# Kernel optimization log

Measured on AMD Instinct MI355X. Metric: run time of the kernel, lower is better.

## Reference

```python
import jax, jax.numpy as jnp
import numpy as np

N, C, H, W = 128, 1024, 16, 16
D_IN, L, D_OUT, NQ = 2048, 512, 1024, 16


def setup_inputs() -> dict:
    key = jax.random.key(0)
    k1, k2, k3, k4, k5 = jax.random.split(key, 5)
    return {
        "cat_tensor": jax.random.normal(k1, (N, C, H, W), dtype=jnp.float32),
        "context": jax.random.normal(k2, (N, D_IN, L), dtype=jnp.float32),
        "query": jax.random.normal(k3, (1, NQ, D_IN), dtype=jnp.float32),
        "W_in": jax.random.normal(k4, (D_IN, D_IN), dtype=jnp.float32) * (1.0 / np.sqrt(D_IN)),
        "W_out": jax.random.normal(k5, (D_OUT, 2 * D_IN), dtype=jnp.float32) * (1.0 / np.sqrt(2 * D_IN)),
    }


def reference(cat_tensor, context, query, W_in, W_out):
    n, c, h, w = cat_tensor.shape
    # AttnBlock: context comes in as [N, D_in, L] -> transpose to [N, L, D_in]
    ctx = jnp.swapaxes(context, 1, 2)  # [N, L, D]
    # learned query broadcast over batch, then 'general' projection (Linear, no bias)
    q = jnp.einsum('nqd,ed->nqe', jnp.broadcast_to(query, (n,) + query.shape[1:]), W_in)  # [N, Q, D]
    scores = jnp.einsum('nqd,nld->nql', q, ctx)            # [N, Q, L]
    weights = jax.nn.softmax(scores, axis=-1)              # [N, Q, L]
    mix = jnp.einsum('nql,nld->nqd', weights, ctx)         # [N, Q, D]
    combined = jnp.concatenate([mix, q], axis=-1)          # [N, Q, 2D]
    out = jnp.tanh(jnp.einsum('nqe,oe->nqo', combined, W_out))  # [N, Q, D_out]
    # reshape queries to a small spatial map: [N, D_out, Hq, Hq]
    hq = int(np.sqrt(out.shape[1]))
    amap = jnp.swapaxes(out, 1, 2).reshape(n, out.shape[2], hq, hq)
    # F.interpolate(..., (H, W)) default mode='nearest': idx = floor(i * in / out)
    ih = (jnp.arange(h) * hq) // h
    iw = (jnp.arange(w) * hq) // w
    amap = amap[:, :, ih, :][:, :, :, iw]                  # [N, D_out, H, W]
    return jnp.concatenate([cat_tensor, amap], axis=1)     # [N, C + D_out, H, W]
```

## Files before the change

### kernel.cpp

```cpp
#include <hip/hip_runtime.h>
#include <hip/hip_bf16.h>

#define NB   128
#define CIN  1024
#define HW   256
#define DIN  2048
#define LL   512
#define DOUT 1024
#define NQ   16

typedef __attribute__((ext_vector_type(8))) short bf16x8;
typedef __attribute__((ext_vector_type(4))) float f32x4;

__global__ __launch_bounds__(256) void k_q(const float* __restrict__ query,
                                           const float* __restrict__ Win,
                                           float* __restrict__ qT) {
  int idx  = blockIdx.x * 4 + (threadIdx.x >> 6);
  int lane = threadIdx.x & 63;
  int e = idx >> 4, qi = idx & 15;
  const float* wr = Win + (size_t)e * DIN;
  const float* qr = query + (size_t)qi * DIN;
  float acc = 0.f;
  for (int d = lane; d < DIN; d += 64) acc += wr[d] * qr[d];
  #pragma unroll
  for (int m = 32; m; m >>= 1) acc += __shfl_xor(acc, m);
  if (lane == 0) qT[e * 16 + qi] = acc;
}

__global__ __launch_bounds__(256) void k_qfill(const float* __restrict__ qT,
                                               __hip_bfloat16* __restrict__ comb) {
  int idx = blockIdx.x * 256 + threadIdx.x;
  int m = idx >> 11, e = idx & 2047;
  comb[(size_t)m * (2 * DIN) + DIN + e] = __float2bfloat16(qT[e * 16 + (m & 15)]);
}

__global__ __launch_bounds__(256) void k_wcast(const float* __restrict__ W,
                                               __hip_bfloat16* __restrict__ Wb) {
  int idx = blockIdx.x * 256 + threadIdx.x;
  Wb[idx] = __float2bfloat16(W[idx]);
}

__global__ __launch_bounds__(256) void k_scores(const float* __restrict__ ctx,
                                                const float* __restrict__ qT,
                                                float* __restrict__ part) {
  int n = blockIdx.x, c = blockIdx.y, t = threadIdx.x;
  const float* cn  = ctx + (size_t)n * DIN * LL + (size_t)c * 512 * LL;
  const float* qTc = qT + (size_t)c * 512 * 16;
  float2 acc[16];
  #pragma unroll
  for (int qi = 0; qi < 16; ++qi) acc[qi] = make_float2(0.f, 0.f);
  #pragma unroll 4
  for (int d = 0; d < 512; ++d) {
    float2 v = *(const float2*)&cn[(size_t)d * LL + 2 * t];
    const float* qr = qTc + d * 16;
    #pragma unroll
    for (int qi = 0; qi < 16; ++qi) {
      acc[qi].x += qr[qi] * v.x;
      acc[qi].y += qr[qi] * v.y;
    }
  }
  float* po = part + (size_t)(c * NB + n) * 16 * LL;
  #pragma unroll
  for (int qi = 0; qi < 16; ++qi)
    *(float2*)&po[qi * LL + 2 * t] = acc[qi];
}

__global__ __launch_bounds__(256) void k_softmax(const float* __restrict__ part,
                                                 float* __restrict__ wT) {
  int b = blockIdx.x, n = b >> 4, qi = b & 15, t = threadIdx.x;
  __shared__ float red[256];
  float sc0 = 0.f, sc1 = 0.f;
  #pragma unroll
  for (int c = 0; c < 4; ++c) {
    const float* p = part + ((size_t)(c * NB + n) * 16 + qi) * LL;
    sc0 += p[t];
    sc1 += p[t + 256];
  }
  red[t] = fmaxf(sc0, sc1);
  __syncthreads();
  for (int s = 128; s; s >>= 1) { if (t < s) red[t] = fmaxf(red[t], red[t + s]); __syncthreads(); }
  float M = red[0];
  __syncthreads();
  float e0 = expf(sc0 - M), e1 = expf(sc1 - M);
  red[t] = e0 + e1;
  __syncthreads();
  for (int s = 128; s; s >>= 1) { if (t < s) red[t] += red[t + s]; __syncthreads(); }
  float inv = 1.0f / red[0];
  wT[((size_t)n * LL + t) * 16 + qi]       = e0 * inv;
  wT[((size_t)n * LL + t + 256) * 16 + qi] = e1 * inv;
}

__global__ __launch_bounds__(256) void k_mix(const float* __restrict__ ctx,
                                             const float* __restrict__ wT,
                                             __hip_bfloat16* __restrict__ comb) {
  int dt = blockIdx.x, n = blockIdx.y, t = threadIdx.x;
  int dbase = dt * 256;
  __shared__ float tile[256 * 33];
  const float* cn = ctx + (size_t)n * DIN * LL;
  const float* wn = wT + (size_t)n * LL * 16;
  float acc[16];
  #pragma unroll
  for (int qi = 0; qi < 16; ++qi) acc[qi] = 0.f;

  for (int ch = 0; ch < 16; ++ch) {
    int l0 = ch * 32;
    __syncthreads();
    int lq = (t & 7) * 4;
    #pragma unroll
    for (int p = 0; p < 8; ++p) {
      int row = (t >> 3) + p * 32;
      float4 g = *(const float4*)&cn[(size_t)(dbase + row) * LL + l0 + lq];
      float* dst = &tile[row * 33 + lq];
      dst[0] = g.x; dst[1] = g.y; dst[2] = g.z; dst[3] = g.w;
    }
    __syncthreads();
    for (int l = 0; l < 32; ++l) {
      float v = tile[t * 33 + l];
      const float* wr = wn + (size_t)(l0 + l) * 16;
      #pragma unroll
      for (int qi = 0; qi < 16; ++qi) acc[qi] += wr[qi] * v;
    }
  }
  #pragma unroll
  for (int qi = 0; qi < 16; ++qi)
    comb[(size_t)(n * 16 + qi) * (2 * DIN) + dbase + t] = __float2bfloat16(acc[qi]);
}

__global__ __launch_bounds__(256) void k_gemm(const __hip_bfloat16* __restrict__ A,
                                              const __hip_bfloat16* __restrict__ B,
                                              float* __restrict__ out) {
  __shared__ short la[64 * 40];
  __shared__ short lb[64 * 40];
  int t = threadIdx.x, lane = t & 63, wid = t >> 6;
  int m0 = blockIdx.y * 64, o0 = blockIdx.x * 64;
  int wy = wid >> 1, wx = wid & 1;
  f32x4 acc[2][2] = {};
  int srow = t >> 2, sq = (t & 3) * 8;
  const short* As = (const short*)A;
  const short* Bs = (const short*)B;

  for (int kc = 0; kc < 2 * DIN; kc += 32) {
    __syncthreads();
    *(float4*)&la[srow * 40 + sq] = *(const float4*)&As[(size_t)(m0 + srow) * (2 * DIN) + kc + sq];
    *(float4*)&lb[srow * 40 + sq] = *(const float4*)&Bs[(size_t)(o0 + srow) * (2 * DIN) + kc + sq];
    __syncthreads();
    int fr = lane & 15, fq = (lane >> 4) * 8;
    bf16x8 a0 = *(const bf16x8*)&la[(wy * 32 + fr) * 40 + fq];
    bf16x8 a1 = *(const bf16x8*)&la[(wy * 32 + 16 + fr) * 40 + fq];
    bf16x8 b0 = *(const bf16x8*)&lb[(wx * 32 + fr) * 40 + fq];
    bf16x8 b1 = *(const bf16x8*)&lb[(wx * 32 + 16 + fr) * 40 + fq];
    acc[0][0] = __builtin_amdgcn_mfma_f32_16x16x32_bf16(a0, b0, acc[0][0], 0, 0, 0);
    acc[0][1] = __builtin_amdgcn_mfma_f32_16x16x32_bf16(a0, b1, acc[0][1], 0, 0, 0);
    acc[1][0] = __builtin_amdgcn_mfma_f32_16x16x32_bf16(a1, b0, acc[1][0], 0, 0, 0);
    acc[1][1] = __builtin_amdgcn_mfma_f32_16x16x32_bf16(a1, b1, acc[1][1], 0, 0, 0);
  }

  int col = lane & 15, rbase = (lane >> 4) * 4;
  #pragma unroll
  for (int si = 0; si < 2; ++si)
    #pragma unroll
    for (int sj = 0; sj < 2; ++sj)
      #pragma unroll
      for (int r = 0; r < 4; ++r) {
        int m = m0 + wy * 32 + si * 16 + rbase + r;
        int o = o0 + wx * 32 + sj * 16 + col;
        float v = tanhf(acc[si][sj][r]);
        int n = m >> 4, qi = m & 15;
        float* op = out + (size_t)(n * 2048 + CIN + o) * HW
                        + ((qi >> 2) * 4) * 16 + (qi & 3) * 4;
        float4 vv = make_float4(v, v, v, v);
        *(float4*)&op[0]  = vv;
        *(float4*)&op[16] = vv;
        *(float4*)&op[32] = vv;
        *(float4*)&op[48] = vv;
      }
}

__global__ __launch_bounds__(256) void k_copy(const float* __restrict__ cat,
                                              float* __restrict__ out) {
  size_t idx = (size_t)blockIdx.x * 256 + threadIdx.x;
  int n = (int)(idx >> 16);
  int rem = (int)(idx & 65535);
  const float4* c4 = (const float4*)cat;
  float4* o4 = (float4*)out;
  o4[(size_t)n * 131072 + rem] = c4[idx];
}

extern "C" void kernel_launch(void* const* d_in, const int* in_sizes, int n_in,
                              void* d_out, int out_size, void* d_ws, size_t ws_size,
                              hipStream_t stream) {
  const float* cat   = (const float*)d_in[0];
  const float* ctx   = (const float*)d_in[1];
  const float* query = (const float*)d_in[2];
  const float* W_in  = (const float*)d_in[3];
  const float* W_out = (const float*)d_in[4];
  float* out = (float*)d_out;

  float* qT   = (float*)d_ws;
  float* wT   = qT + 32768;
  float* part = wT + 1048576;
  __hip_bfloat16* Wb   = (__hip_bfloat16*)(part + 4194304);
  __hip_bfloat16* comb = Wb + 4194304;

  k_q      <<<8192, 256, 0, stream>>>(query, W_in, qT);
  k_wcast  <<<16384, 256, 0, stream>>>(W_out, Wb);
  k_qfill  <<<16384, 256, 0, stream>>>(qT, comb);
  k_scores <<<dim3(128, 4), 256, 0, stream>>>(ctx, qT, part);
  k_softmax<<<2048, 256, 0, stream>>>(part, wT);
  k_mix    <<<dim3(8, 128), 256, 0, stream>>>(ctx, wT, comb);
  k_gemm   <<<dim3(16, 32), 256, 0, stream>>>(comb, Wb, out);
  k_copy   <<<32768, 256, 0, stream>>>(cat, out);
}
```

Baseline: 1.145 ms.

## Vectorize prep kernels, split scores over more chunks, prefetch tiles in mix and GEMM

k_q now computes all 16 queries per warp so each W_in row is read once, and k_wcast/k_qfill write eight bf16 values per thread with vector stores. k_scores splits the D reduction into 8 chunks instead of 4, doubling the block count for better occupancy at the cost of a larger partial-score buffer and more work in softmax. k_mix and k_gemm register-prefetch the next global tile while computing on the current LDS tile, overlapping load latency with math. Workspace offsets are adjusted for the larger partial buffer.

```diff
diff --git a/kernel.cpp b/kernel.cpp
--- a/kernel.cpp
+++ b/kernel.cpp
@@ -9,48 +9,71 @@
 #define DOUT 1024
 #define NQ   16
 
+#define SC   8
+
 typedef __attribute__((ext_vector_type(8))) short bf16x8;
 typedef __attribute__((ext_vector_type(4))) float f32x4;
 
 __global__ __launch_bounds__(256) void k_q(const float* __restrict__ query,
                                            const float* __restrict__ Win,
                                            float* __restrict__ qT) {
-  int idx  = blockIdx.x * 4 + (threadIdx.x >> 6);
+  int e    = blockIdx.x * 4 + (threadIdx.x >> 6);
   int lane = threadIdx.x & 63;
-  int e = idx >> 4, qi = idx & 15;
   const float* wr = Win + (size_t)e * DIN;
-  const float* qr = query + (size_t)qi * DIN;
-  float acc = 0.f;
-  for (int d = lane; d < DIN; d += 64) acc += wr[d] * qr[d];
-  #pragma unroll
-  for (int m = 32; m; m >>= 1) acc += __shfl_xor(acc, m);
-  if (lane == 0) qT[e * 16 + qi] = acc;
+  float acc[16];
+  #pragma unroll
+  for (int qi = 0; qi < 16; ++qi) acc[qi] = 0.f;
+  #pragma unroll 2
+  for (int d = lane; d < DIN; d += 64) {
+    float w = wr[d];
+    #pragma unroll
+    for (int qi = 0; qi < 16; ++qi) acc[qi] += w * query[qi * DIN + d];
+  }
+  #pragma unroll
+  for (int qi = 0; qi < 16; ++qi) {
+    float a = acc[qi];
+    #pragma unroll
+    for (int m = 32; m; m >>= 1) a += __shfl_xor(a, m);
+    if (lane == 0) qT[e * 16 + qi] = a;
+  }
 }
 
 __global__ __launch_bounds__(256) void k_qfill(const float* __restrict__ qT,
                                                __hip_bfloat16* __restrict__ comb) {
   int idx = blockIdx.x * 256 + threadIdx.x;
-  int m = idx >> 11, e = idx & 2047;
-  comb[(size_t)m * (2 * DIN) + DIN + e] = __float2bfloat16(qT[e * 16 + (m & 15)]);
+  int m = idx >> 8, e0 = (idx & 255) * 8;
+  int qi = m & 15;
+  union { bf16x8 v; __hip_bfloat16 h[8]; } u;
+  #pragma unroll
+  for (int j = 0; j < 8; ++j) u.h[j] = __float2bfloat16(qT[(e0 + j) * 16 + qi]);
+  *(bf16x8*)&comb[(size_t)m * (2 * DIN) + DIN + e0] = u.v;
 }
 
 __global__ __launch_bounds__(256) void k_wcast(const float* __restrict__ W,
                                                __hip_bfloat16* __restrict__ Wb) {
   int idx = blockIdx.x * 256 + threadIdx.x;
-  Wb[idx] = __float2bfloat16(W[idx]);
+  const float4* W4 = (const float4*)W;
+  float4 a = W4[idx * 2], b = W4[idx * 2 + 1];
+  union { bf16x8 v; __hip_bfloat16 h[8]; } u;
+  u.h[0] = __float2bfloat16(a.x); u.h[1] = __float2bfloat16(a.y);
+  u.h[2] = __float2bfloat16(a.z); u.h[3] = __float2bfloat16(a.w);
+  u.h[4] = __float2bfloat16(b.x); u.h[5] = __float2bfloat16(b.y);
+  u.h[6] = __float2bfloat16(b.z); u.h[7] = __float2bfloat16(b.w);
+  *(bf16x8*)&Wb[(size_t)idx * 8] = u.v;
 }
 
 __global__ __launch_bounds__(256) void k_scores(const float* __restrict__ ctx,
                                                 const float* __restrict__ qT,
                                                 float* __restrict__ part) {
   int n = blockIdx.x, c = blockIdx.y, t = threadIdx.x;
-  const float* cn  = ctx + (size_t)n * DIN * LL + (size_t)c * 512 * LL;
-  const float* qTc = qT + (size_t)c * 512 * 16;
+  const int DS = DIN / SC;
+  const float* cn  = ctx + (size_t)n * DIN * LL + (size_t)c * DS * LL;
+  const float* qTc = qT + (size_t)c * DS * 16;
   float2 acc[16];
   #pragma unroll
   for (int qi = 0; qi < 16; ++qi) acc[qi] = make_float2(0.f, 0.f);
   #pragma unroll 4
-  for (int d = 0; d < 512; ++d) {
+  for (int d = 0; d < DS; ++d) {
     float2 v = *(const float2*)&cn[(size_t)d * LL + 2 * t];
     const float* qr = qTc + d * 16;
     #pragma unroll
@@ -71,7 +94,7 @@
   __shared__ float red[256];
   float sc0 = 0.f, sc1 = 0.f;
   #pragma unroll
-  for (int c = 0; c < 4; ++c) {
+  for (int c = 0; c < SC; ++c) {
     const float* p = part + ((size_t)(c * NB + n) * 16 + qi) * LL;
     sc0 += p[t];
     sc1 += p[t + 256];
@@ -98,22 +121,35 @@
   __shared__ float tile[256 * 33];
   const float* cn = ctx + (size_t)n * DIN * LL;
   const float* wn = wT + (size_t)n * LL * 16;
+  const float* src0 = cn + (size_t)dbase * LL;
   float acc[16];
   #pragma unroll
   for (int qi = 0; qi < 16; ++qi) acc[qi] = 0.f;
 
+  int lq = (t & 7) * 4;
+  int row0 = t >> 3;
+
+  float4 g[8];
+  #pragma unroll
+  for (int p = 0; p < 8; ++p)
+    g[p] = *(const float4*)&src0[(size_t)(row0 + p * 32) * LL + lq];
+
   for (int ch = 0; ch < 16; ++ch) {
+    __syncthreads();
+    #pragma unroll
+    for (int p = 0; p < 8; ++p) {
+      int row = row0 + p * 32;
+      float* dst = &tile[row * 33 + lq];
+      dst[0] = g[p].x; dst[1] = g[p].y; dst[2] = g[p].z; dst[3] = g[p].w;
+    }
+    __syncthreads();
+    if (ch < 15) {
+      int l0n = (ch + 1) * 32;
+      #pragma unroll
+      for (int p = 0; p < 8; ++p)
+        g[p] = *(const float4*)&src0[(size_t)(row0 + p * 32) * LL + l0n + lq];
+    }
     int l0 = ch * 32;
-    __syncthreads();
-    int lq = (t & 7) * 4;
-    #pragma unroll
-    for (int p = 0; p < 8; ++p) {
-      int row = (t >> 3) + p * 32;
-      float4 g = *(const float4*)&cn[(size_t)(dbase + row) * LL + l0 + lq];
-      float* dst = &tile[row * 33 + lq];
-      dst[0] = g.x; dst[1] = g.y; dst[2] = g.z; dst[3] = g.w;
-    }
-    __syncthreads();
     for (int l = 0; l < 32; ++l) {
       float v = tile[t * 33 + l];
       const float* wr = wn + (size_t)(l0 + l) * 16;
@@ -139,11 +175,18 @@
   const short* As = (const short*)A;
   const short* Bs = (const short*)B;
 
+  float4 ga = *(const float4*)&As[(size_t)(m0 + srow) * (2 * DIN) + sq];
+  float4 gb = *(const float4*)&Bs[(size_t)(o0 + srow) * (2 * DIN) + sq];
+
   for (int kc = 0; kc < 2 * DIN; kc += 32) {
     __syncthreads();
-    *(float4*)&la[srow * 40 + sq] = *(const float4*)&As[(size_t)(m0 + srow) * (2 * DIN) + kc + sq];
-    *(float4*)&lb[srow * 40 + sq] = *(const float4*)&Bs[(size_t)(o0 + srow) * (2 * DIN) + kc + sq];
-    __syncthreads();
+    *(float4*)&la[srow * 40 + sq] = ga;
+    *(float4*)&lb[srow * 40 + sq] = gb;
+    __syncthreads();
+    if (kc + 32 < 2 * DIN) {
+      ga = *(const float4*)&As[(size_t)(m0 + srow) * (2 * DIN) + kc + 32 + sq];
+      gb = *(const float4*)&Bs[(size_t)(o0 + srow) * (2 * DIN) + kc + 32 + sq];
+    }
     int fr = lane & 15, fq = (lane >> 4) * 8;
     bf16x8 a0 = *(const bf16x8*)&la[(wy * 32 + fr) * 40 + fq];
     bf16x8 a1 = *(const bf16x8*)&la[(wy * 32 + 16 + fr) * 40 + fq];
@@ -199,13 +242,13 @@
   float* qT   = (float*)d_ws;
   float* wT   = qT + 32768;
   float* part = wT + 1048576;
-  __hip_bfloat16* Wb   = (__hip_bfloat16*)(part + 4194304);
+  __hip_bfloat16* Wb   = (__hip_bfloat16*)(part + 8388608);
   __hip_bfloat16* comb = Wb + 4194304;
 
-  k_q      <<<8192, 256, 0, stream>>>(query, W_in, qT);
-  k_wcast  <<<16384, 256, 0, stream>>>(W_out, Wb);
-  k_qfill  <<<16384, 256, 0, stream>>>(qT, comb);
-  k_scores <<<dim3(128, 4), 256, 0, stream>>>(ctx, qT, part);
+  k_q      <<<512, 256, 0, stream>>>(query, W_in, qT);
+  k_wcast  <<<2048, 256, 0, stream>>>(W_out, Wb);
+  k_qfill  <<<2048, 256, 0, stream>>>(qT, comb);
+  k_scores <<<dim3(128, SC), 256, 0, stream>>>(ctx, qT, part);
   k_softmax<<<2048, 256, 0, stream>>>(part, wT);
   k_mix    <<<dim3(8, 128), 256, 0, stream>>>(ctx, wT, comb);
   k_gemm   <<<dim3(16, 32), 256, 0, stream>>>(comb, Wb, out);
```

Result: faster. 1.093 ms (-4.5%).
